# Performance work log

Measured on AMD Instinct MI355X. Metric: run time of the kernel, lower is better.

The kernel has to match this reference:

```python
import jax, jax.numpy as jnp
import numpy as np

MATRIX_DIM = 128
FEAT = MATRIX_DIM * (MATRIX_DIM + 1) // 2  # 8256, triu incl. diagonal
HID = FEAT // 5                            # 1651
BATCH = 4096


def setup_inputs() -> dict:
    key = jax.random.key(0)
    k0, k1, k2, k3, k4 = jax.random.split(key, 5)
    stdv1 = 1.0 / FEAT / 2.0
    stdv2 = 1.0 / HID / 2.0
    return {
        "sim_matrices": jax.random.normal(k0, (BATCH, MATRIX_DIM, MATRIX_DIM), dtype=jnp.float32),
        "W1": jax.random.uniform(k1, (HID, FEAT), minval=-stdv1, maxval=stdv1, dtype=jnp.float32),
        "b1": jax.random.uniform(k2, (HID,), minval=-stdv1, maxval=stdv1, dtype=jnp.float32),
        "W2": jax.random.uniform(k3, (1, HID), minval=-stdv2, maxval=stdv2, dtype=jnp.float32),
        "b2": jax.random.uniform(k4, (1,), minval=-stdv2, maxval=stdv2, dtype=jnp.float32),
    }


def reference(sim_matrices, W1, b1, W2, b2):
    # flatten: take upper-triangular (incl. diag) entries -> [B, FEAT]
    iu0, iu1 = np.triu_indices(sim_matrices.shape[1])
    x = sim_matrices[:, iu0, iu1]
    # Linear_block 1 (ideal crossbar VMM = W x + b) + ReLU
    h = jax.nn.relu(jnp.einsum("bf,hf->bh", x, W1) + b1)
    # Linear_block 2 + Sigmoid -> [B, 1]
    return jax.nn.sigmoid(jnp.einsum("bh,oh->bo", h, W2) + b2)
```

## Files before the change

### kernel.cpp

```cpp
#include <hip/hip_runtime.h>
#include <hip/hip_bf16.h>
#include <math.h>

#define MDIM  128
#define FEAT  8256
#define HID   1651
#define HIDP  1664
#define BATCH 4096
#define BK    64
#define KT_TOTAL 129
#define W1SCALE 8192.0f
#define W1INV   (1.0f / 8192.0f)
#define DEPTH 3

using f32x4  = __attribute__((ext_vector_type(4))) float;
using f32x16 = __attribute__((ext_vector_type(16))) float;
using i32x4  = __attribute__((ext_vector_type(4))) int;
using i32x8  = __attribute__((ext_vector_type(8))) int;
typedef long long i64;

__device__ __forceinline__ void gload_lds16(const void* g, void* l) {
    __builtin_amdgcn_global_load_lds(
        (const __attribute__((address_space(1))) void*)g,
        (__attribute__((address_space(3))) void*)l,
        16, 0, 0);
}

__device__ __forceinline__ int row_off(int i) { return (i * (257 - i)) >> 1; }

__device__ __forceinline__ void pack8_fp8(const float* f, int* o) {
    int lo = __builtin_amdgcn_cvt_pk_fp8_f32(f[0], f[1], 0, false);
    lo     = __builtin_amdgcn_cvt_pk_fp8_f32(f[2], f[3], lo, true);
    int hi = __builtin_amdgcn_cvt_pk_fp8_f32(f[4], f[5], 0, false);
    hi     = __builtin_amdgcn_cvt_pk_fp8_f32(f[6], f[7], hi, true);
    o[0] = lo; o[1] = hi;
}

__global__ void __launch_bounds__(256)
prep_kernel(const float* __restrict__ sim, const float* __restrict__ W1,
            char* __restrict__ X, char* __restrict__ W1p,
            float* __restrict__ out_pre) {
    const int t = threadIdx.x;
    if (blockIdx.x < BATCH) {
        const int b = blockIdx.x;
        const float* srow = sim + ((i64)b << 14);
        char* dst = X + (i64)b * FEAT;
#pragma unroll
        for (int it = 0; it < 5; ++it) {
            const int w = it * 256 + t;
            if (w < FEAT / 8) {
                const int f0 = w * 8;
                int i = (int)((257.0f - sqrtf(66049.0f - 8.0f * (float)f0)) * 0.5f);
                i = i < 0 ? 0 : (i > 127 ? 127 : i);
                while (i < 127 && row_off(i + 1) <= f0) ++i;
                while (i > 0 && row_off(i) > f0) --i;
                int j = i + (f0 - row_off(i));
                float v[8];
#pragma unroll
                for (int e = 0; e < 8; ++e) {
                    if (j > 127) { ++i; j = i; }
                    v[e] = srow[i * MDIM + j];
                    ++j;
                }
                int o[2];
                pack8_fp8(v, o);
                *(int2*)(dst + f0) = make_int2(o[0], o[1]);
            }
        }
    } else if (blockIdx.x < BATCH + 5 * HIDP) {
        const int c  = blockIdx.x - BATCH;
        const int wb = c % 5;
        const int n  = c / 5;
        const int w  = wb * 256 + t;
        if (w >= FEAT / 8) return;
        const int f0 = w * 8;
        int o[2];
        if (n < HID) {
            const float* src = W1 + (i64)n * FEAT + f0;
            const f32x4 a = *(const f32x4*)src;
            const f32x4 d = *(const f32x4*)(src + 4);
            float v[8];
#pragma unroll
            for (int e = 0; e < 4; ++e) {
                v[e]     = a[e] * W1SCALE;
                v[e + 4] = d[e] * W1SCALE;
            }
            pack8_fp8(v, o);
        } else {
            o[0] = 0; o[1] = 0;
        }
        *(int2*)(W1p + (i64)n * FEAT + f0) = make_int2(o[0], o[1]);
    } else {
        const f32x4 zz = {0.f, 0.f, 0.f, 0.f};
        f32x4* p = (f32x4*)out_pre + t * 4;
        p[0] = zz; p[1] = zz; p[2] = zz; p[3] = zz;
    }
}

__global__ void __launch_bounds__(256, 3)
gemm_fused_kernel(const char* __restrict__ X,
                  const char* __restrict__ W1p,
                  const float* __restrict__ b1,
                  const float* __restrict__ W2,
                  float* __restrict__ out_pre) {
    __shared__ __align__(16) char lds_a[DEPTH * 8192];
    __shared__ __align__(16) char lds_b[DEPTH * 8192];

    const int t    = threadIdx.x;
    const int w    = t >> 6;
    const int l    = t & 63;
    const int bm   = blockIdx.x;
    const int bn   = blockIdx.y;
    const int wm   = w >> 1;
    const int wn   = w & 1;
    const int lm   = l & 31;
    const int c0   = (l >> 5) << 1;

    f32x16 acc[2][2];
#pragma unroll
    for (int r = 0; r < 16; ++r) {
        acc[0][0][r] = 0.f; acc[0][1][r] = 0.f;
        acc[1][0][r] = 0.f; acc[1][1][r] = 0.f;
    }

    const int nkt = KT_TOTAL;

    const int stR = ((w & 1) << 6) + l;
    const char* gA0 = X + (i64)(bm * 128 + stR) * FEAT + (w >> 1) * 16;
    const char* gB0 = W1p + (i64)(bn * 128 + stR) * FEAT + (w >> 1) * 16;
    char* lA = lds_a + w * 1024;
    char* lB = lds_b + w * 1024;

#define STAGE(buf, kidx) do {                                      \
        const char* _ga = gA0 + (i64)(kidx) * BK;                  \
        const char* _gb = gB0 + (i64)(kidx) * BK;                  \
        char* _la = lA + (buf) * 8192;                             \
        char* _lb = lB + (buf) * 8192;                             \
        gload_lds16(_ga,      _la);                                \
        gload_lds16(_ga + 32, _la + 4096);                         \
        gload_lds16(_gb,      _lb);                                \
        gload_lds16(_gb + 32, _lb + 4096);                         \
    } while (0)

    STAGE(0, 0);
    STAGE(1, 1);
    STAGE(2, 2);

    int cur = 0;
    for (int kt = 0; kt < nkt; ++kt) {
        if (kt + 3 <= nkt)      asm volatile("s_waitcnt vmcnt(8)" ::: "memory");
        else if (kt + 2 == nkt) asm volatile("s_waitcnt vmcnt(4)" ::: "memory");
        else                    asm volatile("s_waitcnt vmcnt(0)" ::: "memory");
        __builtin_amdgcn_s_barrier();
        __builtin_amdgcn_sched_barrier(0);

        const char* pa = lds_a + cur * 8192 + c0 * 2048 + (wm * 64 + lm) * 16;
        const char* pb = lds_b + cur * 8192 + c0 * 2048 + (wn * 64 + lm) * 16;
        i32x8 A0, A1, B0, B1;
        *((i32x4*)&A0)     = *(const i32x4*)(pa);
        *((i32x4*)&A0 + 1) = *(const i32x4*)(pa + 2048);
        *((i32x4*)&A1)     = *(const i32x4*)(pa + 512);
        *((i32x4*)&A1 + 1) = *(const i32x4*)(pa + 512 + 2048);
        *((i32x4*)&B0)     = *(const i32x4*)(pb);
        *((i32x4*)&B0 + 1) = *(const i32x4*)(pb + 2048);
        *((i32x4*)&B1)     = *(const i32x4*)(pb + 512);
        *((i32x4*)&B1 + 1) = *(const i32x4*)(pb + 512 + 2048);

        __builtin_amdgcn_s_setprio(1);
        acc[0][0] = __builtin_amdgcn_mfma_scale_f32_32x32x64_f8f6f4(
            A0, B0, acc[0][0], 0, 0, 0, 0x7F7F7F7F, 0, 0x7F7F7F7F);
        acc[0][1] = __builtin_amdgcn_mfma_scale_f32_32x32x64_f8f6f4(
            A0, B1, acc[0][1], 0, 0, 0, 0x7F7F7F7F, 0, 0x7F7F7F7F);
        acc[1][0] = __builtin_amdgcn_mfma_scale_f32_32x32x64_f8f6f4(
            A1, B0, acc[1][0], 0, 0, 0, 0x7F7F7F7F, 0, 0x7F7F7F7F);
        acc[1][1] = __builtin_amdgcn_mfma_scale_f32_32x32x64_f8f6f4(
            A1, B1, acc[1][1], 0, 0, 0, 0x7F7F7F7F, 0, 0x7F7F7F7F);
        __builtin_amdgcn_s_setprio(0);

        asm volatile("s_waitcnt lgkmcnt(0)" ::: "memory");
        __builtin_amdgcn_sched_barrier(0);
        __builtin_amdgcn_s_barrier();
        __builtin_amdgcn_sched_barrier(0);

        if (kt + 3 < nkt) STAGE(cur, kt + 3);
        cur = (cur == DEPTH - 1) ? 0 : cur + 1;
    }
#undef STAGE

    const int colbase = bn * 128 + wn * 64 + lm;
    float b1v[2], w2v[2];
#pragma unroll
    for (int cb = 0; cb < 2; ++cb) {
        const int col = colbase + cb * 32;
        const bool ok = col < HID;
        b1v[cb] = ok ? b1[col] : 0.f;
        w2v[cb] = ok ? W2[col] : 0.f;
    }
    const int rbase = bm * 128 + wm * 64 + ((l >> 5) << 2);
#pragma unroll
    for (int rb = 0; rb < 2; ++rb)
#pragma unroll
        for (int reg = 0; reg < 16; ++reg) {
            float v = 0.f;
#pragma unroll
            for (int cb = 0; cb < 2; ++cb) {
                const float pre = acc[rb][cb][reg] * W1INV + b1v[cb];
                v += fmaxf(pre, 0.f) * w2v[cb];
            }
            v += __shfl_xor(v, 1);
            v += __shfl_xor(v, 2);
            v += __shfl_xor(v, 4);
            v += __shfl_xor(v, 8);
            v += __shfl_xor(v, 16);
            if (lm == 0) {
                const int row = rbase + rb * 32 + (reg & 3) + ((reg >> 2) << 3);
                atomicAdd(out_pre + row, v);
            }
        }
}

__global__ void __launch_bounds__(256)
sigmoid_kernel(const float* __restrict__ pre,
               const float* __restrict__ b2,
               float* __restrict__ out) {
    const int i = blockIdx.x * 256 + threadIdx.x;
    out[i] = 1.0f / (1.0f + expf(-(pre[i] + b2[0])));
}

extern "C" void kernel_launch(void* const* d_in, const int* in_sizes, int n_in,
                              void* d_out, int out_size, void* d_ws, size_t ws_size,
                              hipStream_t stream) {
    const float* sim = (const float*)d_in[0];
    const float* W1  = (const float*)d_in[1];
    const float* b1  = (const float*)d_in[2];
    const float* W2  = (const float*)d_in[3];
    const float* b2  = (const float*)d_in[4];
    float* out = (float*)d_out;

    char* ws = (char*)d_ws;
    const i64 X_OFF   = 0;
    const i64 W1P_OFF = (i64)BATCH * FEAT;
    const i64 PRE_OFF = W1P_OFF + (i64)HIDP * FEAT;
    char*  Xf8  = ws + X_OFF;
    char*  W1f8 = ws + W1P_OFF;
    float* pre  = (float*)(ws + PRE_OFF);

    prep_kernel<<<BATCH + 5 * HIDP + 1, 256, 0, stream>>>(sim, W1, Xf8, W1f8, pre);
    {
        dim3 grid(BATCH / 128, HIDP / 128);
        gemm_fused_kernel<<<grid, 256, 0, stream>>>(Xf8, W1f8, b1, W2, pre);
    }
    sigmoid_kernel<<<BATCH / 256, 256, 0, stream>>>(pre, b2, out);
}
```

Measured before the change: 501.9 us.

## Store FP8 operands in chunk-major layout for contiguous GEMM tile loads

```diff
diff --git a/kernel.cpp b/kernel.cpp
--- a/kernel.cpp
+++ b/kernel.cpp
@@ -9,9 +9,13 @@
 #define BATCH 4096
 #define BK    64
 #define KT_TOTAL 129
+#define NCHUNK 516
 #define W1SCALE 8192.0f
 #define W1INV   (1.0f / 8192.0f)
 #define DEPTH 3
+
+#define XT_CSTRIDE  ((i64)BATCH * 16)
+#define W1T_CSTRIDE ((i64)HIDP * 16)
 
 using f32x4  = __attribute__((ext_vector_type(4))) float;
 using f32x16 = __attribute__((ext_vector_type(16))) float;
@@ -38,18 +42,17 @@
 
 __global__ void __launch_bounds__(256)
 prep_kernel(const float* __restrict__ sim, const float* __restrict__ W1,
-            char* __restrict__ X, char* __restrict__ W1p,
+            char* __restrict__ Xt, char* __restrict__ W1t,
             float* __restrict__ out_pre) {
     const int t = threadIdx.x;
     if (blockIdx.x < BATCH) {
         const int b = blockIdx.x;
         const float* srow = sim + ((i64)b << 14);
-        char* dst = X + (i64)b * FEAT;
 #pragma unroll
         for (int it = 0; it < 5; ++it) {
-            const int w = it * 256 + t;
-            if (w < FEAT / 8) {
-                const int f0 = w * 8;
+            const int g = it * 256 + t;
+            if (g < FEAT / 8) {
+                const int f0 = g * 8;
                 int i = (int)((257.0f - sqrtf(66049.0f - 8.0f * (float)f0)) * 0.5f);
                 i = i < 0 ? 0 : (i > 127 ? 127 : i);
                 while (i < 127 && row_off(i + 1) <= f0) ++i;
@@ -64,16 +67,17 @@
                 }
                 int o[2];
                 pack8_fp8(v, o);
-                *(int2*)(dst + f0) = make_int2(o[0], o[1]);
+                *(int2*)(Xt + (i64)(g >> 1) * XT_CSTRIDE + (i64)b * 16
+                            + (g & 1) * 8) = make_int2(o[0], o[1]);
             }
         }
     } else if (blockIdx.x < BATCH + 5 * HIDP) {
         const int c  = blockIdx.x - BATCH;
         const int wb = c % 5;
         const int n  = c / 5;
-        const int w  = wb * 256 + t;
-        if (w >= FEAT / 8) return;
-        const int f0 = w * 8;
+        const int g  = wb * 256 + t;
+        if (g >= FEAT / 8) return;
+        const int f0 = g * 8;
         int o[2];
         if (n < HID) {
             const float* src = W1 + (i64)n * FEAT + f0;
@@ -89,7 +93,8 @@
         } else {
             o[0] = 0; o[1] = 0;
         }
-        *(int2*)(W1p + (i64)n * FEAT + f0) = make_int2(o[0], o[1]);
+        *(int2*)(W1t + (i64)(g >> 1) * W1T_CSTRIDE + (i64)n * 16
+                    + (g & 1) * 8) = make_int2(o[0], o[1]);
     } else {
         const f32x4 zz = {0.f, 0.f, 0.f, 0.f};
         f32x4* p = (f32x4*)out_pre + t * 4;
@@ -98,8 +103,8 @@
 }
 
 __global__ void __launch_bounds__(256, 3)
-gemm_fused_kernel(const char* __restrict__ X,
-                  const char* __restrict__ W1p,
+gemm_fused_kernel(const char* __restrict__ Xt,
+                  const char* __restrict__ W1t,
                   const float* __restrict__ b1,
                   const float* __restrict__ W2,
                   float* __restrict__ out_pre) {
@@ -125,21 +130,22 @@
 
     const int nkt = KT_TOTAL;
 
-    const int stR = ((w & 1) << 6) + l;
-    const char* gA0 = X + (i64)(bm * 128 + stR) * FEAT + (w >> 1) * 16;
-    const char* gB0 = W1p + (i64)(bn * 128 + stR) * FEAT + (w >> 1) * 16;
+    const char* gA0 = Xt + (i64)(w >> 1) * XT_CSTRIDE
+                         + ((i64)bm * 128 + (w & 1) * 64 + l) * 16;
+    const char* gB0 = W1t + (i64)(w >> 1) * W1T_CSTRIDE
+                          + ((i64)bn * 128 + (w & 1) * 64 + l) * 16;
     char* lA = lds_a + w * 1024;
     char* lB = lds_b + w * 1024;
 
-#define STAGE(buf, kidx) do {                                      \
-        const char* _ga = gA0 + (i64)(kidx) * BK;                  \
-        const char* _gb = gB0 + (i64)(kidx) * BK;                  \
-        char* _la = lA + (buf) * 8192;                             \
-        char* _lb = lB + (buf) * 8192;                             \
-        gload_lds16(_ga,      _la);                                \
-        gload_lds16(_ga + 32, _la + 4096);                         \
-        gload_lds16(_gb,      _lb);                                \
-        gload_lds16(_gb + 32, _lb + 4096);                         \
+#define STAGE(buf, kidx) do {                                             \
+        const char* _ga = gA0 + (i64)(kidx) * (4 * XT_CSTRIDE);           \
+        const char* _gb = gB0 + (i64)(kidx) * (4 * W1T_CSTRIDE);          \
+        char* _la = lA + (buf) * 8192;                                    \
+        char* _lb = lB + (buf) * 8192;                                    \
+        gload_lds16(_ga,                    _la);                         \
+        gload_lds16(_ga + 2 * XT_CSTRIDE,   _la + 4096);                  \
+        gload_lds16(_gb,                    _lb);                         \
+        gload_lds16(_gb + 2 * W1T_CSTRIDE,  _lb + 4096);                  \
     } while (0)
 
     STAGE(0, 0);
@@ -241,14 +247,14 @@
     const i64 X_OFF   = 0;
     const i64 W1P_OFF = (i64)BATCH * FEAT;
     const i64 PRE_OFF = W1P_OFF + (i64)HIDP * FEAT;
-    char*  Xf8  = ws + X_OFF;
-    char*  W1f8 = ws + W1P_OFF;
+    char*  Xt   = ws + X_OFF;
+    char*  W1t  = ws + W1P_OFF;
     float* pre  = (float*)(ws + PRE_OFF);
 
-    prep_kernel<<<BATCH + 5 * HIDP + 1, 256, 0, stream>>>(sim, W1, Xf8, W1f8, pre);
+    prep_kernel<<<BATCH + 5 * HIDP + 1, 256, 0, stream>>>(sim, W1, Xt, W1t, pre);
     {
         dim3 grid(BATCH / 128, HIDP / 128);
-        gemm_fused_kernel<<<grid, 256, 0, stream>>>(Xf8, W1f8, b1, W2, pre);
+        gemm_fused_kernel<<<grid, 256, 0, stream>>>(Xt, W1t, b1, W2, pre);
     }
     sigmoid_kernel<<<BATCH / 256, 256, 0, stream>>>(pre, b2, out);
 }
```

Measured after the change: 482.8 us. 1.04x faster.
